# Kernel optimization log

Hardware: AMD Instinct MI355X
Metric: run time of the kernel (lower is better)

## Reference

```python
import jax, jax.numpy as jnp
import numpy as np

EPS = 1e-6
NUM_HEADS = 16

def rmsnorm(x, w):
    # x: [..., d], w: [d]
    norm = jax.lax.rsqrt(jnp.mean(x * x, axis=-1, keepdims=True) + EPS)
    return w * (x * norm)

def setup_inputs() -> dict:
    key = jax.random.key(0)
    ks = jax.random.split(key, 6)
    B, N, C = 2, 2048, 1024
    H = NUM_HEADS
    hd = C // H
    x = jax.random.normal(ks[0], (B, N, C), dtype=jnp.float32)
    scale = 1.0 / np.sqrt(C)
    qkv_w = jax.random.normal(ks[1], (C, 3 * C), dtype=jnp.float32) * scale
    qkv_b = jnp.zeros((3 * C,), dtype=jnp.float32)
    q_norm_w = jnp.ones((hd,), dtype=jnp.float32)
    k_norm_w = jnp.ones((hd,), dtype=jnp.float32)
    proj_w = jax.random.normal(ks[2], (C, C), dtype=jnp.float32) * scale
    proj_b = jnp.zeros((C,), dtype=jnp.float32)
    return {"x": x, "qkv_w": qkv_w, "qkv_b": qkv_b,
            "q_norm_w": q_norm_w, "k_norm_w": k_norm_w,
            "proj_w": proj_w, "proj_b": proj_b}

def reference(x, qkv_w, qkv_b, q_norm_w, k_norm_w, proj_w, proj_b):
    B, N, C = x.shape
    H = NUM_HEADS
    hd = C // H
    qkv = x @ qkv_w + qkv_b                       # [B,N,3C]
    qkv = qkv.reshape(B, N, 3, H, hd)
    q, k, v = qkv[:, :, 0], qkv[:, :, 1], qkv[:, :, 2]  # [B,N,H,hd]
    q = jnp.transpose(q, (0, 2, 1, 3))            # [B,H,N,hd]
    k = jnp.transpose(k, (0, 2, 1, 3))
    v = jnp.transpose(v, (0, 2, 1, 3))
    q = rmsnorm(q, q_norm_w)
    k = rmsnorm(k, k_norm_w)
    scores = jnp.einsum('bhqd,bhkd->bhqk', q, k) / jnp.sqrt(jnp.float32(hd))
    attn = jax.nn.softmax(scores, axis=-1)
    out = jnp.einsum('bhqk,bhkd->bhqd', attn, v)  # [B,H,N,hd]
    out = jnp.transpose(out, (0, 2, 1, 3)).reshape(B, N, C)
    return out @ proj_w + proj_b
```

## Files before the change

### kernel.cpp

```cpp
#include <hip/hip_runtime.h>

typedef unsigned short u16;
typedef unsigned int u32;
typedef __bf16 bf16x8 __attribute__((ext_vector_type(8)));
typedef float f32x4 __attribute__((ext_vector_type(4)));
typedef unsigned short u16x8 __attribute__((ext_vector_type(8)));
typedef unsigned short u16x4 __attribute__((ext_vector_type(4)));

__device__ __forceinline__ float bf2f(u16 u) {
    union { unsigned int i; float f; } c; c.i = ((unsigned int)u) << 16; return c.f;
}
__device__ __forceinline__ u16 f2bf(float f) {
    union { float f; unsigned int i; } c; c.f = f;
    unsigned int r = c.i + 0x7FFFu + ((c.i >> 16) & 1u);
    return (u16)(r >> 16);
}
__device__ __forceinline__ u16 f2bf_rtz(float f) {
    union { float f; unsigned int i; } c; c.f = f;
    return (u16)(c.i >> 16);
}
__device__ __forceinline__ float fast_exp2(float x) {
#if __has_builtin(__builtin_amdgcn_exp2f)
    return __builtin_amdgcn_exp2f(x);
#else
    return exp2f(x);
#endif
}
__device__ __forceinline__ bf16x8 u2b(u16x8 v) {
    return __builtin_bit_cast(bf16x8, v);
}
__device__ __forceinline__ void async16(const void* g, void* l) {
    __builtin_amdgcn_global_load_lds(
        (const __attribute__((address_space(1))) u32*)g,
        (__attribute__((address_space(3))) u32*)l, 16, 0, 0);
}

__global__ __launch_bounds__(256) void prep(
    const float* __restrict__ X, u16* __restrict__ Xb,
    const float* __restrict__ qkv_w, u16* __restrict__ qwT,
    const float* __restrict__ proj_w, u16* __restrict__ pwT)
{
    __shared__ float tile[32][33];
    const int blk = blockIdx.x;
    const int t = threadIdx.x;
    if (blk < 2048) {
        const size_t i = ((size_t)blk * 256 + t) * 8;
        u16x8 h;
        #pragma unroll
        for (int e = 0; e < 8; ++e) h[e] = f2bf(X[i + e]);
        *(u16x8*)&Xb[i] = h;
        return;
    }
    const float* W; u16* Th; int K, N, bx, by;
    if (blk < 5120) {
        W = qkv_w; Th = qwT; K = 1024; N = 3072;
        bx = (blk - 2048) % 96; by = (blk - 2048) / 96;
    } else {
        W = proj_w; Th = pwT; K = 1024; N = 1024;
        bx = (blk - 5120) % 32; by = (blk - 5120) / 32;
    }
    const int bk = by * 32, bn = bx * 32;
    const int tx = t & 31, ty = t >> 5;
    #pragma unroll
    for (int r = ty; r < 32; r += 8)
        tile[r][tx] = W[(size_t)(bk + r) * N + bn + tx];
    __syncthreads();
    #pragma unroll
    for (int r = ty; r < 32; r += 8)
        Th[(size_t)(bn + r) * K + bk + tx] = f2bf(tile[tx][r]);
}

__global__ __launch_bounds__(256) void gemm_qkv(
    const u16* __restrict__ AH, const u16* __restrict__ BH,
    const float* __restrict__ bias,
    u16* __restrict__ Qb, u16* __restrict__ Kb, u16* __restrict__ Vt,
    const float* __restrict__ qw, const float* __restrict__ kw)
{
    const int K = 1024;
    __shared__ __align__(16) u16 AhT[128 * 32];
    __shared__ __align__(16) u16 BhT[128 * 32];
    const int t = threadIdx.x;
    const int bm = blockIdx.y * 128, bn = blockIdx.x * 128;
    const int wave = t >> 6, lane = t & 63;
    const int wm = (wave >> 1) * 64, wn = (wave & 1) * 64;
    const int l15 = lane & 15, quad = lane >> 4;
    const int srow = lane >> 2, scol = (lane & 3) * 8;

    f32x4 acc[4][4];
    const f32x4 zero = {0.0f, 0.0f, 0.0f, 0.0f};
    #pragma unroll
    for (int i = 0; i < 4; ++i)
        #pragma unroll
        for (int j = 0; j < 4; ++j) acc[i][j] = zero;

    for (int k0 = 0; k0 < K; k0 += 32) {
        #pragma unroll
        for (int rr = 0; rr < 2; ++rr) {
            const int r0 = (rr * 4 + wave) * 16;
            const size_t ga = (size_t)(bm + r0 + srow) * K + k0 + scol;
            const size_t gb = (size_t)(bn + r0 + srow) * K + k0 + scol;
            async16(&AH[ga], &AhT[r0 * 32]);
            async16(&BH[gb], &BhT[r0 * 32]);
        }
        __syncthreads();
        bf16x8 ah[4], bh[4];
        #pragma unroll
        for (int i = 0; i < 4; ++i)
            ah[i] = *(const bf16x8*)&AhT[(wm + i * 16 + l15) * 32 + quad * 8];
        #pragma unroll
        for (int j = 0; j < 4; ++j)
            bh[j] = *(const bf16x8*)&BhT[(wn + j * 16 + l15) * 32 + quad * 8];
        #pragma unroll
        for (int i = 0; i < 4; ++i)
            #pragma unroll
            for (int j = 0; j < 4; ++j)
                acc[i][j] = __builtin_amdgcn_mfma_f32_16x16x32_bf16(
                    ah[i], bh[j], acc[i][j], 0, 0, 0);
        __syncthreads();
    }

    const int gc0 = bn + wn;
    const int sec = gc0 >> 10;
    const int h = (gc0 & 1023) >> 6;
    const int b = bm >> 11;
    const int bhd = b * 16 + h;
    float bv[4], wj[4];
    #pragma unroll
    for (int j = 0; j < 4; ++j) {
        const int d = j * 16 + l15;
        bv[j] = bias[gc0 + d];
        wj[j] = (sec == 2) ? 0.0f : (sec ? kw[d] : qw[d] * 0.18033688011f);
    }
    if (sec < 2) {
        u16* dst = sec ? Kb : Qb;
        #pragma unroll
        for (int i = 0; i < 4; ++i) {
            float val[4][4];
            float ss[4] = {0.0f, 0.0f, 0.0f, 0.0f};
            #pragma unroll
            for (int j = 0; j < 4; ++j)
                #pragma unroll
                for (int r = 0; r < 4; ++r) {
                    val[j][r] = acc[i][j][r] + bv[j];
                    ss[r] += val[j][r] * val[j][r];
                }
            #pragma unroll
            for (int r = 0; r < 4; ++r) {
                #pragma unroll
                for (int m = 1; m < 16; m <<= 1)
                    ss[r] += __shfl_xor(ss[r], m, 64);
                const float nrm = rsqrtf(ss[r] * 0.015625f + 1e-6f);
                const int n = (bm + wm + i * 16 + quad * 4 + r) & 2047;
                const size_t rowb = ((size_t)bhd * 2048 + n) * 64;
                #pragma unroll
                for (int j = 0; j < 4; ++j)
                    dst[rowb + j * 16 + l15] = f2bf(val[j][r] * nrm * wj[j]);
            }
        }
    } else {
        const int nb = (bm + wm) & 2047;
        #pragma unroll
        for (int i = 0; i < 4; ++i) {
            const int s0 = (i & 1) * 32 + quad * 8 + (i >> 1) * 4;
            #pragma unroll
            for (int j = 0; j < 4; ++j) {
                const int d = j * 16 + l15;
                u16x4 pk;
                #pragma unroll
                for (int r = 0; r < 4; ++r)
                    pk[r] = f2bf(acc[i][j][r] + bv[j]);
                *(u16x4*)&Vt[((size_t)bhd * 64 + d) * 2048 + nb + s0] = pk;
            }
        }
    }
}

__global__ __launch_bounds__(256) void gemm_proj(
    const u16* __restrict__ AH, const u16* __restrict__ BH,
    const float* __restrict__ bias, float* __restrict__ C)
{
    const int N = 1024, K = 1024;
    __shared__ __align__(16) u16 AhT[64 * 32];
    __shared__ __align__(16) u16 BhT[128 * 32];
    const int t = threadIdx.x;
    const int bm = blockIdx.y * 64, bn = blockIdx.x * 128;
    const int wave = t >> 6, lane = t & 63;
    const int l15 = lane & 15, quad = lane >> 4;
    const int srow = lane >> 2, scol = (lane & 3) * 8;

    f32x4 acc[4][2];
    const f32x4 zero = {0.0f, 0.0f, 0.0f, 0.0f};
    #pragma unroll
    for (int i = 0; i < 4; ++i)
        #pragma unroll
        for (int j = 0; j < 2; ++j) acc[i][j] = zero;

    for (int k0 = 0; k0 < K; k0 += 32) {
        {
            const int r0 = wave * 16;
            async16(&AH[(size_t)(bm + r0 + srow) * K + k0 + scol],
                    &AhT[r0 * 32]);
        }
        #pragma unroll
        for (int cc = 0; cc < 2; ++cc) {
            const int r0 = (wave * 2 + cc) * 16;
            async16(&BH[(size_t)(bn + r0 + srow) * K + k0 + scol],
                    &BhT[r0 * 32]);
        }
        __syncthreads();
        bf16x8 ah[4], bh[2];
        #pragma unroll
        for (int i = 0; i < 4; ++i)
            ah[i] = *(const bf16x8*)&AhT[(i * 16 + l15) * 32 + quad * 8];
        #pragma unroll
        for (int j = 0; j < 2; ++j)
            bh[j] = *(const bf16x8*)
                &BhT[(wave * 32 + j * 16 + l15) * 32 + quad * 8];
        #pragma unroll
        for (int i = 0; i < 4; ++i)
            #pragma unroll
            for (int j = 0; j < 2; ++j)
                acc[i][j] = __builtin_amdgcn_mfma_f32_16x16x32_bf16(
                    ah[i], bh[j], acc[i][j], 0, 0, 0);
        __syncthreads();
    }

    #pragma unroll
    for (int j = 0; j < 2; ++j) {
        const int col = bn + wave * 32 + j * 16 + l15;
        const float bv = bias[col];
        #pragma unroll
        for (int i = 0; i < 4; ++i) {
            const int row = bm + i * 16 + quad * 4;
            #pragma unroll
            for (int r = 0; r < 4; ++r)
                C[(size_t)(row + r) * N + col] = acc[i][j][r] + bv;
        }
    }
}

__global__ __launch_bounds__(256) void flash_attn_mfma(
    const u16* __restrict__ Qb, const u16* __restrict__ Kb,
    const u16* __restrict__ Vt, u16* __restrict__ Attn)
{
    __shared__ __align__(16) u16 Klds[2 * 64 * 64];
    __shared__ __align__(16) u16 Vlds[2 * 64 * 64];
    __shared__ float Lbuf[128];

    const int t = threadIdx.x;
    const int bid = blockIdx.x;
    const int bh = bid & 31;
    const int qt = bid >> 5;
    const int n0 = qt * 128;
    const size_t kbase = (size_t)bh * 2048 * 64;
    const size_t vbase = (size_t)bh * 64 * 2048;
    const int wave = t >> 6, lane = t & 63;
    const int l15 = lane & 15, quad = lane >> 4;
    const int srow8 = lane >> 3;
    const int sgrp = lane & 7;

    bf16x8 qf[2][2];
    #pragma unroll
    for (int qs = 0; qs < 2; ++qs) {
        const size_t qrow =
            ((size_t)bh * 2048 + n0 + wave * 32 + qs * 16 + l15) * 64;
        qf[qs][0] = *(const bf16x8*)&Qb[qrow + quad * 8];
        qf[qs][1] = *(const bf16x8*)&Qb[qrow + 32 + quad * 8];
    }

    int kofs[4][2];
    #pragma unroll
    for (int nt = 0; nt < 4; ++nt) {
        const int row = nt * 16 + l15;
        kofs[nt][0] = row * 64 + ((quad ^ (row & 7)) * 8);
        kofs[nt][1] = row * 64 + (((quad + 4) ^ (row & 7)) * 8);
    }

    f32x4 o[2][4];
    const f32x4 zero = {0.0f, 0.0f, 0.0f, 0.0f};
    #pragma unroll
    for (int qs = 0; qs < 2; ++qs)
        #pragma unroll
        for (int dt = 0; dt < 4; ++dt) o[qs][dt] = zero;
    float lsum[2] = {0.0f, 0.0f};

    #pragma unroll
    for (int cc = 0; cc < 2; ++cc) {
        const int r0 = (wave + cc * 4) * 8;
        const int row = r0 + srow8;
        const int gg = sgrp ^ (row & 7);
        async16(&Kb[kbase + (size_t)row * 64 + gg * 8], &Klds[r0 * 64]);
        async16(&Vt[vbase + (size_t)row * 2048 + gg * 8], &Vlds[r0 * 64]);
    }

    for (int kt = 0; kt < 32; ++kt) {
        __syncthreads();
        if (kt + 1 < 32) {
            const int nb = ((kt + 1) & 1) * 4096;
            #pragma unroll
            for (int cc = 0; cc < 2; ++cc) {
                const int r0 = (wave + cc * 4) * 8;
                const int row = r0 + srow8;
                const int gg = sgrp ^ (row & 7);
                async16(&Kb[kbase + (size_t)((kt + 1) * 64 + row) * 64 + gg * 8],
                        &Klds[nb + r0 * 64]);
                async16(&Vt[vbase + (size_t)row * 2048 + (kt + 1) * 64 + gg * 8],
                        &Vlds[nb + r0 * 64]);
            }
        }
        const int cb = (kt & 1) * 4096;

        f32x4 s[2][4];
        #pragma unroll
        for (int nt = 0; nt < 4; ++nt) {
            bf16x8 kf0 = *(const bf16x8*)&Klds[cb + kofs[nt][0]];
            bf16x8 kf1 = *(const bf16x8*)&Klds[cb + kofs[nt][1]];
            __builtin_amdgcn_s_setprio(1);
            #pragma unroll
            for (int qs = 0; qs < 2; ++qs) {
                s[qs][nt] = zero;
                s[qs][nt] = __builtin_amdgcn_mfma_f32_16x16x32_bf16(
                    kf0, qf[qs][0], s[qs][nt], 0, 0, 0);
                s[qs][nt] = __builtin_amdgcn_mfma_f32_16x16x32_bf16(
                    kf1, qf[qs][1], s[qs][nt], 0, 0, 0);
            }
            __builtin_amdgcn_s_setprio(0);
        }

        bf16x8 pf[2][2];
        #pragma unroll
        for (int qs = 0; qs < 2; ++qs) {
            #pragma unroll
            for (int m = 0; m < 2; ++m) {
                u16x8 pk;
                #pragma unroll
                for (int r = 0; r < 4; ++r) {
                    const float p0 = fast_exp2(s[qs][m][r]);
                    lsum[qs] += p0;
                    pk[r] = f2bf_rtz(p0);
                    const float p1 = fast_exp2(s[qs][m + 2][r]);
                    lsum[qs] += p1;
                    pk[4 + r] = f2bf_rtz(p1);
                }
                pf[qs][m] = u2b(pk);
            }
        }

        #pragma unroll
        for (int dt = 0; dt < 4; ++dt) {
            bf16x8 vf0 = *(const bf16x8*)&Vlds[cb + kofs[dt][0]];
            bf16x8 vf1 = *(const bf16x8*)&Vlds[cb + kofs[dt][1]];
            __builtin_amdgcn_s_setprio(1);
            #pragma unroll
            for (int qs = 0; qs < 2; ++qs) {
                o[qs][dt] = __builtin_amdgcn_mfma_f32_16x16x32_bf16(
                    pf[qs][0], vf0, o[qs][dt], 0, 0, 0);
                o[qs][dt] = __builtin_amdgcn_mfma_f32_16x16x32_bf16(
                    pf[qs][1], vf1, o[qs][dt], 0, 0, 0);
            }
            __builtin_amdgcn_s_setprio(0);
        }
    }

    #pragma unroll
    for (int qs = 0; qs < 2; ++qs) {
        lsum[qs] += __shfl_xor(lsum[qs], 16, 64);
        lsum[qs] += __shfl_xor(lsum[qs], 32, 64);
        if (quad == 0) Lbuf[wave * 32 + qs * 16 + l15] = lsum[qs];
    }
    __syncthreads();
    const size_t obase =
        ((size_t)(bh >> 4) * 2048 + n0) * 1024 + (bh & 15) * 64;
    #pragma unroll
    for (int qs = 0; qs < 2; ++qs)
        #pragma unroll
        for (int r = 0; r < 4; ++r) {
            const float inv =
                1.0f / Lbuf[wave * 32 + qs * 16 + quad * 4 + r];
            const size_t rbase =
                obase + (size_t)(wave * 32 + qs * 16 + quad * 4 + r) * 1024;
            #pragma unroll
            for (int dt = 0; dt < 4; ++dt)
                Attn[rbase + dt * 16 + l15] = f2bf(o[qs][dt][r] * inv);
        }
}

extern "C" void kernel_launch(void* const* d_in, const int* in_sizes, int n_in,
                              void* d_out, int out_size, void* d_ws, size_t ws_size,
                              hipStream_t stream)
{
    const float* x      = (const float*)d_in[0];
    const float* qkv_w  = (const float*)d_in[1];
    const float* qkv_b  = (const float*)d_in[2];
    const float* q_nw   = (const float*)d_in[3];
    const float* k_nw   = (const float*)d_in[4];
    const float* proj_w = (const float*)d_in[5];
    const float* proj_b = (const float*)d_in[6];
    float* out = (float*)d_out;

    char* ws = (char*)d_ws;
    u16* AttnB = (u16*)ws;
    u16* qwT   = (u16*)(ws + 8388608);
    u16* pwT   = (u16*)(ws + 14680064);
    u16* Xb    = (u16*)(ws + 16777216);
    u16* QbB   = (u16*)(ws + 25165824);
    u16* KbB   = (u16*)(ws + 33554432);
    u16* VtB   = (u16*)(ws + 41943040);
    (void)in_sizes; (void)n_in; (void)out_size;
    if (ws_size < 50331648u) return;

    prep<<<dim3(6144), 256, 0, stream>>>(x, Xb, qkv_w, qwT, proj_w, pwT);
    gemm_qkv<<<dim3(3072 / 128, 4096 / 128), 256, 0, stream>>>(
        Xb, qwT, qkv_b, QbB, KbB, VtB, q_nw, k_nw);
    flash_attn_mfma<<<dim3(512), 256, 0, stream>>>(QbB, KbB, VtB, AttnB);
    gemm_proj<<<dim3(1024 / 128, 4096 / 64), 256, 0, stream>>>(
        AttnB, pwT, proj_b, out);
}
```

Measured before the change: 199.9 us.

## Halve attention query tile per block and compute row sums via MFMA with ones

Each flash-attention block now handles 64 query rows instead of 128, so the grid doubles to 1024 blocks, and each wave processes one 16-row query slice. The softmax denominator is no longer accumulated with scalar adds plus shuffle reductions and an LDS exchange; it comes from an extra MFMA of the probability fragments against a vector of bf16 ones. This targets higher occupancy and parallelism and drops the final barrier, at the cost of loading each K/V tile twice as often overall and halving MFMA reuse of each loaded K/V fragment. The row sum now uses the bf16-rounded probabilities, which slightly changes the numerics.

```diff
diff --git a/kernel.cpp b/kernel.cpp
--- a/kernel.cpp
+++ b/kernel.cpp
@@ -245,13 +245,12 @@
 {
     __shared__ __align__(16) u16 Klds[2 * 64 * 64];
     __shared__ __align__(16) u16 Vlds[2 * 64 * 64];
-    __shared__ float Lbuf[128];
 
     const int t = threadIdx.x;
     const int bid = blockIdx.x;
     const int bh = bid & 31;
     const int qt = bid >> 5;
-    const int n0 = qt * 128;
+    const int n0 = qt * 64;
     const size_t kbase = (size_t)bh * 2048 * 64;
     const size_t vbase = (size_t)bh * 64 * 2048;
     const int wave = t >> 6, lane = t & 63;
@@ -259,13 +258,12 @@
     const int srow8 = lane >> 3;
     const int sgrp = lane & 7;
 
-    bf16x8 qf[2][2];
-    #pragma unroll
-    for (int qs = 0; qs < 2; ++qs) {
+    bf16x8 qf[2];
+    {
         const size_t qrow =
-            ((size_t)bh * 2048 + n0 + wave * 32 + qs * 16 + l15) * 64;
-        qf[qs][0] = *(const bf16x8*)&Qb[qrow + quad * 8];
-        qf[qs][1] = *(const bf16x8*)&Qb[qrow + 32 + quad * 8];
+            ((size_t)bh * 2048 + n0 + wave * 16 + l15) * 64;
+        qf[0] = *(const bf16x8*)&Qb[qrow + quad * 8];
+        qf[1] = *(const bf16x8*)&Qb[qrow + 32 + quad * 8];
     }
 
     int kofs[4][2];
@@ -276,13 +274,14 @@
         kofs[nt][1] = row * 64 + (((quad + 4) ^ (row & 7)) * 8);
     }
 
-    f32x4 o[2][4];
+    f32x4 o[4];
     const f32x4 zero = {0.0f, 0.0f, 0.0f, 0.0f};
     #pragma unroll
-    for (int qs = 0; qs < 2; ++qs)
-        #pragma unroll
-        for (int dt = 0; dt < 4; ++dt) o[qs][dt] = zero;
-    float lsum[2] = {0.0f, 0.0f};
+    for (int dt = 0; dt < 4; ++dt) o[dt] = zero;
+    f32x4 osum = zero;
+    bf16x8 ones;
+    #pragma unroll
+    for (int e = 0; e < 8; ++e) ones[e] = (__bf16)1.0f;
 
     #pragma unroll
     for (int cc = 0; cc < 2; ++cc) {
@@ -310,40 +309,29 @@
         }
         const int cb = (kt & 1) * 4096;
 
-        f32x4 s[2][4];
+        f32x4 s[4];
         #pragma unroll
         for (int nt = 0; nt < 4; ++nt) {
             bf16x8 kf0 = *(const bf16x8*)&Klds[cb + kofs[nt][0]];
             bf16x8 kf1 = *(const bf16x8*)&Klds[cb + kofs[nt][1]];
             __builtin_amdgcn_s_setprio(1);
-            #pragma unroll
-            for (int qs = 0; qs < 2; ++qs) {
-                s[qs][nt] = zero;
-                s[qs][nt] = __builtin_amdgcn_mfma_f32_16x16x32_bf16(
-                    kf0, qf[qs][0], s[qs][nt], 0, 0, 0);
-                s[qs][nt] = __builtin_amdgcn_mfma_f32_16x16x32_bf16(
-                    kf1, qf[qs][1], s[qs][nt], 0, 0, 0);
+            s[nt] = __builtin_amdgcn_mfma_f32_16x16x32_bf16(
+                kf0, qf[0], zero, 0, 0, 0);
+            s[nt] = __builtin_amdgcn_mfma_f32_16x16x32_bf16(
+                kf1, qf[1], s[nt], 0, 0, 0);
+            __builtin_amdgcn_s_setprio(0);
+        }
+
+        bf16x8 pf[2];
+        #pragma unroll
+        for (int m = 0; m < 2; ++m) {
+            u16x8 pk;
+            #pragma unroll
+            for (int r = 0; r < 4; ++r) {
+                pk[r]     = f2bf_rtz(fast_exp2(s[m][r]));
+                pk[4 + r] = f2bf_rtz(fast_exp2(s[m + 2][r]));
             }
-            __builtin_amdgcn_s_setprio(0);
-        }
-
-        bf16x8 pf[2][2];
-        #pragma unroll
-        for (int qs = 0; qs < 2; ++qs) {
-            #pragma unroll
-            for (int m = 0; m < 2; ++m) {
-                u16x8 pk;
-                #pragma unroll
-                for (int r = 0; r < 4; ++r) {
-                    const float p0 = fast_exp2(s[qs][m][r]);
-                    lsum[qs] += p0;
-                    pk[r] = f2bf_rtz(p0);
-                    const float p1 = fast_exp2(s[qs][m + 2][r]);
-                    lsum[qs] += p1;
-                    pk[4 + r] = f2bf_rtz(p1);
-                }
-                pf[qs][m] = u2b(pk);
-            }
+            pf[m] = u2b(pk);
         }
 
         #pragma unroll
@@ -351,38 +339,31 @@
             bf16x8 vf0 = *(const bf16x8*)&Vlds[cb + kofs[dt][0]];
             bf16x8 vf1 = *(const bf16x8*)&Vlds[cb + kofs[dt][1]];
             __builtin_amdgcn_s_setprio(1);
-            #pragma unroll
-            for (int qs = 0; qs < 2; ++qs) {
-                o[qs][dt] = __builtin_amdgcn_mfma_f32_16x16x32_bf16(
-                    pf[qs][0], vf0, o[qs][dt], 0, 0, 0);
-                o[qs][dt] = __builtin_amdgcn_mfma_f32_16x16x32_bf16(
-                    pf[qs][1], vf1, o[qs][dt], 0, 0, 0);
-            }
+            o[dt] = __builtin_amdgcn_mfma_f32_16x16x32_bf16(
+                pf[0], vf0, o[dt], 0, 0, 0);
+            o[dt] = __builtin_amdgcn_mfma_f32_16x16x32_bf16(
+                pf[1], vf1, o[dt], 0, 0, 0);
             __builtin_amdgcn_s_setprio(0);
         }
-    }
-
-    #pragma unroll
-    for (int qs = 0; qs < 2; ++qs) {
-        lsum[qs] += __shfl_xor(lsum[qs], 16, 64);
-        lsum[qs] += __shfl_xor(lsum[qs], 32, 64);
-        if (quad == 0) Lbuf[wave * 32 + qs * 16 + l15] = lsum[qs];
-    }
-    __syncthreads();
+        __builtin_amdgcn_s_setprio(1);
+        osum = __builtin_amdgcn_mfma_f32_16x16x32_bf16(
+            pf[0], ones, osum, 0, 0, 0);
+        osum = __builtin_amdgcn_mfma_f32_16x16x32_bf16(
+            pf[1], ones, osum, 0, 0, 0);
+        __builtin_amdgcn_s_setprio(0);
+    }
+
     const size_t obase =
         ((size_t)(bh >> 4) * 2048 + n0) * 1024 + (bh & 15) * 64;
     #pragma unroll
-    for (int qs = 0; qs < 2; ++qs)
-        #pragma unroll
-        for (int r = 0; r < 4; ++r) {
-            const float inv =
-                1.0f / Lbuf[wave * 32 + qs * 16 + quad * 4 + r];
-            const size_t rbase =
-                obase + (size_t)(wave * 32 + qs * 16 + quad * 4 + r) * 1024;
-            #pragma unroll
-            for (int dt = 0; dt < 4; ++dt)
-                Attn[rbase + dt * 16 + l15] = f2bf(o[qs][dt][r] * inv);
-        }
+    for (int r = 0; r < 4; ++r) {
+        const float inv = 1.0f / osum[r];
+        const size_t rbase =
+            obase + (size_t)(wave * 16 + quad * 4 + r) * 1024;
+        #pragma unroll
+        for (int dt = 0; dt < 4; ++dt)
+            Attn[rbase + dt * 16 + l15] = f2bf(o[dt][r] * inv);
+    }
 }
 
 extern "C" void kernel_launch(void* const* d_in, const int* in_sizes, int n_in,
@@ -412,7 +393,7 @@
     prep<<<dim3(6144), 256, 0, stream>>>(x, Xb, qkv_w, qwT, proj_w, pwT);
     gemm_qkv<<<dim3(3072 / 128, 4096 / 128), 256, 0, stream>>>(
         Xb, qwT, qkv_b, QbB, KbB, VtB, q_nw, k_nw);
-    flash_attn_mfma<<<dim3(512), 256, 0, stream>>>(QbB, KbB, VtB, AttnB);
+    flash_attn_mfma<<<dim3(1024), 256, 0, stream>>>(QbB, KbB, VtB, AttnB);
     gemm_proj<<<dim3(1024 / 128, 4096 / 64), 256, 0, stream>>>(
         AttnB, pwT, proj_b, out);
 }
```

Measured after the change: 201.6 us. Within noise of the previous version (+0.9%).

## Halve attention block size and compute row sums with MFMA against ones

Applied to the files above, without the earlier changes.

The flash attention kernel now launches 1024 blocks of 128 threads, each covering 64 query rows instead of 128, so the grid doubles and more blocks can be resident per CU. The scalar per-element softmax denominator accumulation, its cross-lane shuffles, the LDS buffer and the barrier are replaced by extra MFMA instructions that multiply the probability tiles by a vector of ones. The row sums then land directly in the output layout. In exchange, the K/V tiles are now loaded twice as often in total across blocks and each wave issues extra matrix instructions. The denominator also uses the bf16-rounded probabilities rather than the fp32 values.

```diff
diff --git a/kernel.cpp b/kernel.cpp
--- a/kernel.cpp
+++ b/kernel.cpp
@@ -239,19 +239,18 @@
     }
 }
 
-__global__ __launch_bounds__(256) void flash_attn_mfma(
+__global__ __launch_bounds__(128) void flash_attn_mfma(
     const u16* __restrict__ Qb, const u16* __restrict__ Kb,
     const u16* __restrict__ Vt, u16* __restrict__ Attn)
 {
     __shared__ __align__(16) u16 Klds[2 * 64 * 64];
     __shared__ __align__(16) u16 Vlds[2 * 64 * 64];
-    __shared__ float Lbuf[128];
 
     const int t = threadIdx.x;
     const int bid = blockIdx.x;
     const int bh = bid & 31;
     const int qt = bid >> 5;
-    const int n0 = qt * 128;
+    const int n0 = qt * 64;
     const size_t kbase = (size_t)bh * 2048 * 64;
     const size_t vbase = (size_t)bh * 64 * 2048;
     const int wave = t >> 6, lane = t & 63;
@@ -282,11 +281,14 @@
     for (int qs = 0; qs < 2; ++qs)
         #pragma unroll
         for (int dt = 0; dt < 4; ++dt) o[qs][dt] = zero;
-    float lsum[2] = {0.0f, 0.0f};
-
-    #pragma unroll
-    for (int cc = 0; cc < 2; ++cc) {
-        const int r0 = (wave + cc * 4) * 8;
+    f32x4 osum[2] = {zero, zero};
+    bf16x8 ones;
+    #pragma unroll
+    for (int e = 0; e < 8; ++e) ones[e] = (__bf16)1.0f;
+
+    #pragma unroll
+    for (int cc = 0; cc < 4; ++cc) {
+        const int r0 = (wave * 4 + cc) * 8;
         const int row = r0 + srow8;
         const int gg = sgrp ^ (row & 7);
         async16(&Kb[kbase + (size_t)row * 64 + gg * 8], &Klds[r0 * 64]);
@@ -298,8 +300,8 @@
         if (kt + 1 < 32) {
             const int nb = ((kt + 1) & 1) * 4096;
             #pragma unroll
-            for (int cc = 0; cc < 2; ++cc) {
-                const int r0 = (wave + cc * 4) * 8;
+            for (int cc = 0; cc < 4; ++cc) {
+                const int r0 = (wave * 4 + cc) * 8;
                 const int row = r0 + srow8;
                 const int gg = sgrp ^ (row & 7);
                 async16(&Kb[kbase + (size_t)((kt + 1) * 64 + row) * 64 + gg * 8],
@@ -318,9 +320,8 @@
             __builtin_amdgcn_s_setprio(1);
             #pragma unroll
             for (int qs = 0; qs < 2; ++qs) {
-                s[qs][nt] = zero;
                 s[qs][nt] = __builtin_amdgcn_mfma_f32_16x16x32_bf16(
-                    kf0, qf[qs][0], s[qs][nt], 0, 0, 0);
+                    kf0, qf[qs][0], zero, 0, 0, 0);
                 s[qs][nt] = __builtin_amdgcn_mfma_f32_16x16x32_bf16(
                     kf1, qf[qs][1], s[qs][nt], 0, 0, 0);
             }
@@ -335,12 +336,8 @@
                 u16x8 pk;
                 #pragma unroll
                 for (int r = 0; r < 4; ++r) {
-                    const float p0 = fast_exp2(s[qs][m][r]);
-                    lsum[qs] += p0;
-                    pk[r] = f2bf_rtz(p0);
-                    const float p1 = fast_exp2(s[qs][m + 2][r]);
-                    lsum[qs] += p1;
-                    pk[4 + r] = f2bf_rtz(p1);
+                    pk[r]     = f2bf_rtz(fast_exp2(s[qs][m][r]));
+                    pk[4 + r] = f2bf_rtz(fast_exp2(s[qs][m + 2][r]));
                 }
                 pf[qs][m] = u2b(pk);
             }
@@ -360,23 +357,24 @@
             }
             __builtin_amdgcn_s_setprio(0);
         }
-    }
-
-    #pragma unroll
-    for (int qs = 0; qs < 2; ++qs) {
-        lsum[qs] += __shfl_xor(lsum[qs], 16, 64);
-        lsum[qs] += __shfl_xor(lsum[qs], 32, 64);
-        if (quad == 0) Lbuf[wave * 32 + qs * 16 + l15] = lsum[qs];
-    }
-    __syncthreads();
+        __builtin_amdgcn_s_setprio(1);
+        #pragma unroll
+        for (int qs = 0; qs < 2; ++qs) {
+            osum[qs] = __builtin_amdgcn_mfma_f32_16x16x32_bf16(
+                pf[qs][0], ones, osum[qs], 0, 0, 0);
+            osum[qs] = __builtin_amdgcn_mfma_f32_16x16x32_bf16(
+                pf[qs][1], ones, osum[qs], 0, 0, 0);
+        }
+        __builtin_amdgcn_s_setprio(0);
+    }
+
     const size_t obase =
         ((size_t)(bh >> 4) * 2048 + n0) * 1024 + (bh & 15) * 64;
     #pragma unroll
     for (int qs = 0; qs < 2; ++qs)
         #pragma unroll
         for (int r = 0; r < 4; ++r) {
-            const float inv =
-                1.0f / Lbuf[wave * 32 + qs * 16 + quad * 4 + r];
+            const float inv = 1.0f / osum[qs][r];
             const size_t rbase =
                 obase + (size_t)(wave * 32 + qs * 16 + quad * 4 + r) * 1024;
             #pragma unroll
@@ -412,7 +410,7 @@
     prep<<<dim3(6144), 256, 0, stream>>>(x, Xb, qkv_w, qwT, proj_w, pwT);
     gemm_qkv<<<dim3(3072 / 128, 4096 / 128), 256, 0, stream>>>(
         Xb, qwT, qkv_b, QbB, KbB, VtB, q_nw, k_nw);
-    flash_attn_mfma<<<dim3(512), 256, 0, stream>>>(QbB, KbB, VtB, AttnB);
+    flash_attn_mfma<<<dim3(1024), 128, 0, stream>>>(QbB, KbB, VtB, AttnB);
     gemm_proj<<<dim3(1024 / 128, 4096 / 64), 256, 0, stream>>>(
         AttnB, pwT, proj_b, out);
 }
```

After: 199.7 us. About the same (-0.1%).
